# Optimization experiments

Measured on AMD Instinct MI355X. Metric: run time of the kernel, lower is better.

## Reference

```python
import jax, jax.numpy as jnp
import numpy as np

NUM_CEPS = 13  # default num_ceps in log_mel_to_cepstral


def _dct_basis(n_mels, num_ceps):
    # Orthonormal DCT-II basis (scipy.fftpack.dct type=2, norm='ortho'),
    # truncated to the first num_ceps rows. Shape (num_ceps, n_mels).
    n = jnp.arange(n_mels, dtype=jnp.float32)
    k = jnp.arange(num_ceps, dtype=jnp.float32)
    basis = jnp.cos(jnp.pi * (n[None, :] + 0.5) * k[:, None] / n_mels)
    scale = jnp.where(k == 0, jnp.sqrt(1.0 / n_mels), jnp.sqrt(2.0 / n_mels))
    return basis * scale[:, None]


def _log_mel_to_cepstral(mel, basis):
    # mel: (B, 1, F, T) -> cepstral (B, num_ceps, T) with CMVN over (B*T)
    x = jnp.log1p(jnp.abs(mel[:, 0]))                 # (B, F, T)
    c = jnp.einsum('kf,bft->bkt', basis, x)           # (B, num_ceps, T)
    mean = jnp.mean(c, axis=(0, 2), keepdims=True)
    # torch .std is unbiased (ddof=1) over the B*T flattened samples
    std = jnp.std(c, axis=(0, 2), keepdims=True, ddof=1) + 1e-6
    return (c - mean) / std


def setup_inputs() -> dict:
    key = jax.random.key(0)
    k1, k2 = jax.random.split(key)
    B, F, T = 64, 128, 4096
    mel_true = jax.random.normal(k1, (B, 1, F, T), dtype=jnp.float32)
    mel_pred = jax.random.normal(k2, (B, 1, F, T), dtype=jnp.float32)
    return {"mel_true": mel_true, "mel_pred": mel_pred}


def reference(mel_true, mel_pred):
    n_mels = mel_true.shape[2]
    basis = _dct_basis(n_mels, NUM_CEPS)
    c_true = _log_mel_to_cepstral(mel_true, basis)
    c_pred = _log_mel_to_cepstral(mel_pred, basis)
    diff = c_true - c_pred
    mse_dist = jnp.sum(diff * diff, axis=1)           # (B, T)
    log_base_10 = 10.0 / jnp.log(jnp.float32(10.0))
    mcd = log_base_10 * jnp.sqrt(2.0 * mse_dist)
    return jnp.mean(mcd)
```

## Files before the change

kernel.cpp:

```cpp
#include <hip/hip_runtime.h>
#include <math.h>

#define BB 64
#define FF 128
#define TT 4096
#define KK 13
#define NT (BB * TT)
#define NPAIR (NT / 2)
#define MCD_C  6.14185100f


#define KLIST(X) X(0) X(1) X(2) X(3) X(4) X(5) X(6) X(7) X(8) X(9) X(10) X(11) X(12)
#define K12(X)        X(1) X(2) X(3) X(4) X(5) X(6) X(7) X(8) X(9) X(10) X(11) X(12)

template <int CTRL>
__device__ __forceinline__ float dpp_add(float x) {
    return x + __int_as_float(__builtin_amdgcn_update_dpp(
                   0, __float_as_int(x), CTRL, 0xf, 0xf, true));
}
__device__ __forceinline__ float wave_sum(float x) {
    x = dpp_add<0x111>(x);
    x = dpp_add<0x112>(x);
    x = dpp_add<0x114>(x);
    x = dpp_add<0x118>(x);
    x = dpp_add<0x142>(x);
    x = dpp_add<0x143>(x);
    return x;
}

__global__ __launch_bounds__(256)
__attribute__((amdgpu_waves_per_eu(8, 8)))
void pass1_kernel(
    const float* __restrict__ melT, const float* __restrict__ melP,
    float* __restrict__ sums, float* __restrict__ cT, float* __restrict__ cP)
{
    const int tensor = blockIdx.x >> 10;
    const int tid  = threadIdx.x;
    const int lane = tid & 63;
    const int wave = tid >> 6;
    const int half = lane >> 5;
    const int gp = (blockIdx.x & 1023) * 128 + wave * 32 + (lane & 31);
    const float* __restrict__ src = tensor ? melP : melT;
    float* __restrict__ dst = tensor ? cP : cT;

    const int g0 = gp << 1;
    const int b  = g0 >> 12;
    const int t0 = g0 & (TT - 1);
    const int fbase = half << 6;
    const float* p = src + (size_t)b * (FF * TT) + (size_t)fbase * TT + t0;

#define DECLACC(i) float ax##i = 0.f, ay##i = 0.f;
    KLIST(DECLACC)
#undef DECLACC

    for (int f0 = 0; f0 < 64; f0 += 8) {
        float2 v[8];
#pragma unroll
        for (int j = 0; j < 8; ++j)
            v[j] = *(const float2*)(p + (size_t)(f0 + j) * TT);

#pragma unroll
        for (int j = 0; j < 8; ++j) {
            const float xx = __log2f(1.0f + fabsf(v[j].x));
            const float xy = __log2f(1.0f + fabsf(v[j].y));

            const float b1 = __cosf((3.14159265358979f / 128.0f) *
                                    ((float)(fbase + f0 + j) + 0.5f));
            const float tw = b1 + b1;
            const float b2  = fmaf(tw, b1,  -1.0f);
            const float b3  = fmaf(tw, b2,  -b1);
            const float b4  = fmaf(tw, b3,  -b2);
            const float b5  = fmaf(tw, b4,  -b3);
            const float b6  = fmaf(tw, b5,  -b4);
            const float b7  = fmaf(tw, b6,  -b5);
            const float b8  = fmaf(tw, b7,  -b6);
            const float b9  = fmaf(tw, b8,  -b7);
            const float b10 = fmaf(tw, b9,  -b8);
            const float b11 = fmaf(tw, b10, -b9);
            const float b12 = fmaf(tw, b11, -b10);

            ax0 += xx; ay0 += xy;
#define FMAK(i) ax##i = fmaf(b##i, xx, ax##i); ay##i = fmaf(b##i, xy, ay##i);
            K12(FMAK)
#undef FMAK
        }
    }

#define MRG(i) ax##i += __shfl_xor(ax##i, 32); ay##i += __shfl_xor(ay##i, 32);
    KLIST(MRG)
#undef MRG

    if (half == 0) {
#define STK(i) ((float2*)(dst + (size_t)(i) * NT))[gp] = make_float2(ax##i, ay##i);
        KLIST(STK)
#undef STK
    }

    __shared__ float red[4][26];
#define REDK(i) { \
        float s = wave_sum(ax##i + ay##i); \
        float q = wave_sum(fmaf(ax##i, ax##i, ay##i * ay##i)); \
        if (lane == 63) { red[wave][i] = s; red[wave][13 + i] = q; } }
    KLIST(REDK)
#undef REDK
    __syncthreads();
    if (tid < 26) {
        const float v = red[0][tid] + red[1][tid] + red[2][tid] + red[3][tid];
        atomicAdd(&sums[(tensor * 26 + tid) * 16], 0.5f * v);
    }
}

__global__ __launch_bounds__(256) void pass2_kernel(
    const float* __restrict__ sums, const float* __restrict__ cT,
    const float* __restrict__ cP, float* __restrict__ out)
{
    __shared__ float mS[2][13], iS[2][13];
    if (threadIdx.x < 26) {
        const int tns = threadIdx.x >= 13;
        const int k   = threadIdx.x - tns * 13;
        const float s = sums[(tns * 26 + k) * 16];
        const float q = sums[(tns * 26 + 13 + k) * 16];
        const float N = (float)NT;
        const float m = s / N;
        const float var = fmaxf((q - s * m) / (N - 1.0f), 0.0f);
        mS[tns][k] = m;
        iS[tns][k] = 1.0f / (sqrtf(var) + 1e-6f);
    }
    __syncthreads();

    const int col = blockIdx.x * 256 + threadIdx.x;
    float ss = 0.0f;
#pragma unroll
    for (int k = 0; k < KK; ++k) {
        const float a = cT[(size_t)k * NT + col];
        const float p = cP[(size_t)k * NT + col];
        const float d = (a - mS[0][k]) * iS[0][k] - (p - mS[1][k]) * iS[1][k];
        ss = fmaf(d, d, ss);
    }
    float v = wave_sum(MCD_C * sqrtf(ss));

    const int lane = threadIdx.x & 63;
    const int wave = threadIdx.x >> 6;
    __shared__ float r2[4];
    if (lane == 63) r2[wave] = v;
    __syncthreads();
    if (threadIdx.x == 0)
        atomicAdd(out, (r2[0] + r2[1] + r2[2] + r2[3]) * (1.0f / (float)NT));
}

extern "C" void kernel_launch(void* const* d_in, const int* in_sizes, int n_in,
                              void* d_out, int out_size, void* d_ws, size_t ws_size,
                              hipStream_t stream) {
    const float* melT = (const float*)d_in[0];
    const float* melP = (const float*)d_in[1];
    float* out  = (float*)d_out;
    float* sums = (float*)d_ws;
    float* cT   = (float*)((char*)d_ws + 8192);
    float* cP   = cT + (size_t)KK * NT;

    hipMemsetAsync(d_ws, 0, 4096, stream);
    hipMemsetAsync(d_out, 0, sizeof(float), stream);

    pass1_kernel<<<2048, 256, 0, stream>>>(melT, melP, sums, cT, cP);
    pass2_kernel<<<1024, 256, 0, stream>>>(sums, cT, cP, out);
}
```

Baseline: 309.4 us.

## Stream mel planes through an LDS ring via async global-to-LDS loads

Pass 1 is restructured so each block covers 1024 time columns of one batch row and streams all 128 mel planes through a 4-deep LDS ring buffer, using global_load_lds with explicit vmcnt waits and barriers. Each thread now keeps 4 columns by 13 accumulators, which removes the cross-half shuffle merge and its 0.5 scaling. The grid drops to 512 blocks at 2 waves per EU, trading occupancy for deeper software prefetch. Barrier overhead and lower occupancy may limit how much memory latency is actually hidden.

```diff
diff --git a/kernel.cpp b/kernel.cpp
--- a/kernel.cpp
+++ b/kernel.cpp
@@ -6,12 +6,16 @@
 #define TT 4096
 #define KK 13
 #define NT (BB * TT)
-#define NPAIR (NT / 2)
 #define MCD_C  6.14185100f
 
+#define CPB 1024
+#define CPT 4
+#define PPB 4
+#define NBATCH (FF / PPB)
+#define RING 4
+
 
 #define KLIST(X) X(0) X(1) X(2) X(3) X(4) X(5) X(6) X(7) X(8) X(9) X(10) X(11) X(12)
-#define K12(X)        X(1) X(2) X(3) X(4) X(5) X(6) X(7) X(8) X(9) X(10) X(11) X(12)
 
 template <int CTRL>
 __device__ __forceinline__ float dpp_add(float x) {
@@ -28,85 +32,124 @@
     return x;
 }
 
+__device__ __forceinline__ void gload_lds16(const float* g, float* l) {
+    __builtin_amdgcn_global_load_lds(
+        (const __attribute__((address_space(1))) void*)g,
+        (__attribute__((address_space(3))) void*)l, 16, 0, 0);
+}
+
+template <int N>
+__device__ __forceinline__ void wait_vm() {
+    asm volatile("s_waitcnt vmcnt(%0)" :: "n"(N) : "memory");
+}
+
 __global__ __launch_bounds__(256)
-__attribute__((amdgpu_waves_per_eu(8, 8)))
+__attribute__((amdgpu_waves_per_eu(2, 2)))
 void pass1_kernel(
     const float* __restrict__ melT, const float* __restrict__ melP,
     float* __restrict__ sums, float* __restrict__ cT, float* __restrict__ cP)
 {
-    const int tensor = blockIdx.x >> 10;
+    __shared__ float ring[RING][PPB][CPB];
+    __shared__ float red[4][26];
+
     const int tid  = threadIdx.x;
     const int lane = tid & 63;
     const int wave = tid >> 6;
-    const int half = lane >> 5;
-    const int gp = (blockIdx.x & 1023) * 128 + wave * 32 + (lane & 31);
+
+    const int tensor = blockIdx.x >> 8;
+    const int idx    = blockIdx.x & 255;
+    const int b      = idx >> 2;
+    const int t0     = (idx & 3) * CPB;
+
     const float* __restrict__ src = tensor ? melP : melT;
     float* __restrict__ dst = tensor ? cP : cT;
 
-    const int g0 = gp << 1;
-    const int b  = g0 >> 12;
-    const int t0 = g0 & (TT - 1);
-    const int fbase = half << 6;
-    const float* p = src + (size_t)b * (FF * TT) + (size_t)fbase * TT + t0;
-
-#define DECLACC(i) float ax##i = 0.f, ay##i = 0.f;
-    KLIST(DECLACC)
-#undef DECLACC
-
-    for (int f0 = 0; f0 < 64; f0 += 8) {
-        float2 v[8];
-#pragma unroll
-        for (int j = 0; j < 8; ++j)
-            v[j] = *(const float2*)(p + (size_t)(f0 + j) * TT);
-
-#pragma unroll
-        for (int j = 0; j < 8; ++j) {
-            const float xx = __log2f(1.0f + fabsf(v[j].x));
-            const float xy = __log2f(1.0f + fabsf(v[j].y));
-
-            const float b1 = __cosf((3.14159265358979f / 128.0f) *
-                                    ((float)(fbase + f0 + j) + 0.5f));
-            const float tw = b1 + b1;
-            const float b2  = fmaf(tw, b1,  -1.0f);
-            const float b3  = fmaf(tw, b2,  -b1);
-            const float b4  = fmaf(tw, b3,  -b2);
-            const float b5  = fmaf(tw, b4,  -b3);
-            const float b6  = fmaf(tw, b5,  -b4);
-            const float b7  = fmaf(tw, b6,  -b5);
-            const float b8  = fmaf(tw, b7,  -b6);
-            const float b9  = fmaf(tw, b8,  -b7);
-            const float b10 = fmaf(tw, b9,  -b8);
-            const float b11 = fmaf(tw, b10, -b9);
-            const float b12 = fmaf(tw, b11, -b10);
-
-            ax0 += xx; ay0 += xy;
-#define FMAK(i) ax##i = fmaf(b##i, xx, ax##i); ay##i = fmaf(b##i, xy, ay##i);
-            K12(FMAK)
-#undef FMAK
+    const float* gsrc = src + (size_t)b * (FF * TT) + t0 + wave * 256 + lane * 4;
+
+    float ac[KK][CPT];
+#pragma unroll
+    for (int k = 0; k < KK; ++k)
+#pragma unroll
+        for (int c = 0; c < CPT; ++c) ac[k][c] = 0.0f;
+
+    auto issue_batch = [&](int bt) {
+        const int slot = bt & (RING - 1);
+#pragma unroll
+        for (int pl = 0; pl < PPB; ++pl) {
+            const int f = bt * PPB + pl;
+            gload_lds16(gsrc + (size_t)f * TT, &ring[slot][pl][wave * 256]);
         }
-    }
-
-#define MRG(i) ax##i += __shfl_xor(ax##i, 32); ay##i += __shfl_xor(ay##i, 32);
-    KLIST(MRG)
-#undef MRG
-
-    if (half == 0) {
-#define STK(i) ((float2*)(dst + (size_t)(i) * NT))[gp] = make_float2(ax##i, ay##i);
-        KLIST(STK)
-#undef STK
-    }
-
-    __shared__ float red[4][26];
-#define REDK(i) { \
-        float s = wave_sum(ax##i + ay##i); \
-        float q = wave_sum(fmaf(ax##i, ax##i, ay##i * ay##i)); \
-        if (lane == 63) { red[wave][i] = s; red[wave][13 + i] = q; } }
-    KLIST(REDK)
-#undef REDK
+    };
+
+    auto compute_batch = [&](int bt) {
+        const int slot = bt & (RING - 1);
+#pragma unroll
+        for (int pl = 0; pl < PPB; ++pl) {
+            const int f = bt * PPB + pl;
+            const float4 v = *(const float4*)&ring[slot][pl][tid * 4];
+            float bk[KK];
+            bk[0] = 1.0f;
+            bk[1] = __cosf((3.14159265358979f / 128.0f) * ((float)f + 0.5f));
+            const float tw = bk[1] + bk[1];
+#pragma unroll
+            for (int k = 2; k < KK; ++k) bk[k] = fmaf(tw, bk[k - 1], -bk[k - 2]);
+            const float x0 = __log2f(1.0f + fabsf(v.x));
+            const float x1 = __log2f(1.0f + fabsf(v.y));
+            const float x2 = __log2f(1.0f + fabsf(v.z));
+            const float x3 = __log2f(1.0f + fabsf(v.w));
+#pragma unroll
+            for (int k = 0; k < KK; ++k) {
+                ac[k][0] = fmaf(bk[k], x0, ac[k][0]);
+                ac[k][1] = fmaf(bk[k], x1, ac[k][1]);
+                ac[k][2] = fmaf(bk[k], x2, ac[k][2]);
+                ac[k][3] = fmaf(bk[k], x3, ac[k][3]);
+            }
+        }
+    };
+
+    issue_batch(0); issue_batch(1); issue_batch(2); issue_batch(3);
+
+    for (int bt = 0; bt <= 28; ++bt) {
+        wait_vm<12>();
+        __builtin_amdgcn_s_barrier();
+        __builtin_amdgcn_sched_barrier(0);
+        compute_batch(bt);
+        __builtin_amdgcn_s_barrier();
+        __builtin_amdgcn_sched_barrier(0);
+        if (bt < 28) issue_batch(bt + 4);
+    }
+    wait_vm<8>();
+    __builtin_amdgcn_s_barrier();
+    __builtin_amdgcn_sched_barrier(0);
+    compute_batch(29);
+    wait_vm<4>();
+    __builtin_amdgcn_s_barrier();
+    __builtin_amdgcn_sched_barrier(0);
+    compute_batch(30);
+    wait_vm<0>();
+    __builtin_amdgcn_s_barrier();
+    __builtin_amdgcn_sched_barrier(0);
+    compute_batch(31);
+
+    const size_t col0 = (size_t)b * TT + t0 + tid * CPT;
+#pragma unroll
+    for (int k = 0; k < KK; ++k)
+        *(float4*)&dst[(size_t)k * NT + col0] =
+            make_float4(ac[k][0], ac[k][1], ac[k][2], ac[k][3]);
+
+#pragma unroll
+    for (int k = 0; k < KK; ++k) {
+        float s = (ac[k][0] + ac[k][1]) + (ac[k][2] + ac[k][3]);
+        float q = fmaf(ac[k][0], ac[k][0], ac[k][1] * ac[k][1]) +
+                  fmaf(ac[k][2], ac[k][2], ac[k][3] * ac[k][3]);
+        s = wave_sum(s);
+        q = wave_sum(q);
+        if (lane == 63) { red[wave][k] = s; red[wave][13 + k] = q; }
+    }
     __syncthreads();
     if (tid < 26) {
         const float v = red[0][tid] + red[1][tid] + red[2][tid] + red[3][tid];
-        atomicAdd(&sums[(tensor * 26 + tid) * 16], 0.5f * v);
+        atomicAdd(&sums[(tensor * 26 + tid) * 16], v);
     }
 }
 
@@ -161,6 +204,6 @@
     hipMemsetAsync(d_ws, 0, 4096, stream);
     hipMemsetAsync(d_out, 0, sizeof(float), stream);
 
-    pass1_kernel<<<2048, 256, 0, stream>>>(melT, melP, sums, cT, cP);
+    pass1_kernel<<<512, 256, 0, stream>>>(melT, melP, sums, cT, cP);
     pass2_kernel<<<1024, 256, 0, stream>>>(sums, cT, cP, out);
 }
```

After: 307.9 us. Within noise of the previous version (-0.5%).
